# Kernel optimization log

Measured on AMD Instinct MI355X. Metric: run time of the kernel, lower is better.

## Reference

```python
import jax, jax.numpy as jnp
import numpy as np

H = 1024      # hidden_size
E = 8         # num_experts
I = 4 * H     # intermediate_size
B, S = 2, 2048


def setup_inputs() -> dict:
    key = jax.random.key(0)
    ks = jax.random.split(key, 7)
    s_h = 1.0 / np.sqrt(H)
    s_i = 1.0 / np.sqrt(I)
    return {
        "x": jax.random.normal(ks[0], (B, S, H), dtype=jnp.float32),
        "gate_w": jax.random.uniform(ks[1], (H, E), jnp.float32, -s_h, s_h),
        "gate_b": jax.random.uniform(ks[2], (E,), jnp.float32, -s_h, s_h),
        "W1": jax.random.uniform(ks[3], (E, H, I), jnp.float32, -s_h, s_h),
        "b1": jax.random.uniform(ks[4], (E, I), jnp.float32, -s_h, s_h),
        "W2": jax.random.uniform(ks[5], (E, I, H), jnp.float32, -s_i, s_i),
        "b2": jax.random.uniform(ks[6], (E, H), jnp.float32, -s_i, s_i),
    }


def reference(x, gate_w, gate_b, W1, b1, W2, b2):
    b, s, h = x.shape
    flat = x.reshape(-1, h)                      # [T, H]
    T = flat.shape[0]
    e = gate_b.shape[0]

    # Router: softmax -> top-2 -> renormalize
    logits = flat @ gate_w + gate_b              # [T, E]
    probs = jax.nn.softmax(logits, axis=-1)
    top_w, top_idx = jax.lax.top_k(probs, 2)     # [T, 2]
    top_w = top_w / (top_w.sum(axis=-1, keepdims=True) + 1e-6)

    # Dense per-token gate weight matrix [T, E] (0 except top-2 slots)
    gate_full = jnp.zeros((T, e), flat.dtype).at[
        jnp.arange(T)[:, None], top_idx
    ].add(top_w)

    # All experts on all tokens (dense, math-equivalent combine via gate_full)
    hmid = jax.nn.gelu(jnp.einsum('th,ehi->eti', flat, W1) + b1[:, None, :],
                       approximate=True)         # [E, T, I]
    y = jnp.einsum('eti,eih->eth', hmid, W2) + b2[:, None, :]  # [E, T, H]
    out = jnp.einsum('te,eth->th', gate_full, y)  # weighted combine
    return out.reshape(b, s, h)
```

## Files before the change

kernel.cpp:

```cpp
#include <hip/hip_runtime.h>
#include <hip/hip_bf16.h>
#include <math.h>

#define H_DIM 1024
#define E_NUM 8
#define I_DIM 4096
#define T_NUM 4096
#define CAP   8192

typedef __attribute__((ext_vector_type(8))) short bf16x8;
typedef __attribute__((ext_vector_type(4))) float f32x4;

__device__ inline unsigned short f2bf(float f) {
  union { __hip_bfloat16 h; unsigned short u; } cv;
  cv.h = __float2bfloat16(f);
  return cv.u;
}

__global__ void router_kernel(const float* __restrict__ x,
                              const float* __restrict__ gw,
                              const float* __restrict__ gb,
                              int* __restrict__ cnt,
                              int* __restrict__ list,
                              float* __restrict__ tokw) {
  const int t = blockIdx.x;
  const int l = threadIdx.x;
  const float* xr = x + (size_t)t * H_DIM;
  float acc[E_NUM];
#pragma unroll
  for (int e = 0; e < E_NUM; ++e) acc[e] = 0.f;
#pragma unroll
  for (int j = 0; j < H_DIM / 64; ++j) {
    const int h = l + j * 64;
    const float xv = xr[h];
    const float4* g = (const float4*)(gw + (size_t)h * E_NUM);
    const float4 g0 = g[0], g1 = g[1];
    acc[0] += xv * g0.x; acc[1] += xv * g0.y; acc[2] += xv * g0.z; acc[3] += xv * g0.w;
    acc[4] += xv * g1.x; acc[5] += xv * g1.y; acc[6] += xv * g1.z; acc[7] += xv * g1.w;
  }
#pragma unroll
  for (int off = 32; off > 0; off >>= 1) {
#pragma unroll
    for (int e = 0; e < E_NUM; ++e) acc[e] += __shfl_down(acc[e], off, 64);
  }
  if (l == 0) {
    float lg[E_NUM], mx = -1e30f;
#pragma unroll
    for (int e = 0; e < E_NUM; ++e) { lg[e] = acc[e] + gb[e]; mx = fmaxf(mx, lg[e]); }
    float p[E_NUM], s = 0.f;
#pragma unroll
    for (int e = 0; e < E_NUM; ++e) { p[e] = expf(lg[e] - mx); s += p[e]; }
    const float inv = 1.f / s;
#pragma unroll
    for (int e = 0; e < E_NUM; ++e) p[e] *= inv;
    int i0 = 0;
#pragma unroll
    for (int e = 1; e < E_NUM; ++e) if (p[e] > p[i0]) i0 = e;
    int i1 = (i0 == 0) ? 1 : 0;
#pragma unroll
    for (int e = 0; e < E_NUM; ++e) if (e != i0 && p[e] > p[i1]) i1 = e;
    const float denom = p[i0] + p[i1] + 1e-6f;
    const float w0 = p[i0] / denom, w1 = p[i1] / denom;
    int pos = atomicAdd(&cnt[i0], 1);
    list[i0 * CAP + pos] = t * 2;
    tokw[t * 2] = w0;
    pos = atomicAdd(&cnt[i1], 1);
    list[i1 * CAP + pos] = t * 2 + 1;
    tokw[t * 2 + 1] = w1;
  }
}

__global__ void scan_kernel(const int* __restrict__ cnt, int* __restrict__ base) {
  if (threadIdx.x == 0 && blockIdx.x == 0) {
    int b = 0;
    for (int e = 0; e < E_NUM; ++e) { base[e] = b; b += cnt[e]; }
  }
}

__launch_bounds__(256)
__global__ void gemm1_kernel(const float* __restrict__ x,
                             const float* __restrict__ W1,
                             const float* __restrict__ b1,
                             const int* __restrict__ cnt,
                             const int* __restrict__ base,
                             const int* __restrict__ list,
                             unsigned short* __restrict__ hmid) {
  const int e = blockIdx.z;
  const int c = cnt[e];
  const int m0 = blockIdx.y * 128;
  if (m0 >= c) return;
  const int n0 = blockIdx.x * 128;

  __shared__ int toks[128];
  __shared__ __align__(16) unsigned short As[128 * 40];
  __shared__ __align__(16) unsigned short Bs[128 * 40];

  const int tid = threadIdx.x;
  if (tid < 128) {
    int idx = m0 + tid; if (idx >= c) idx = c - 1;
    toks[tid] = list[e * CAP + idx] >> 1;
  }
  __syncthreads();

  const int lane = tid & 63;
  const int wave = tid >> 6;
  const int wm = (wave >> 1) * 64;
  const int wn = (wave & 1) * 64;
  const int l16 = lane & 15;
  const int quad = lane >> 4;

  f32x4 acc[16];
#pragma unroll
  for (int i = 0; i < 16; ++i) acc[i] = (f32x4){0.f, 0.f, 0.f, 0.f};

  const float* W1e = W1 + (size_t)e * H_DIM * I_DIM;

  for (int kt = 0; kt < H_DIM / 32; ++kt) {
    const int k0 = kt * 32;
#pragma unroll
    for (int i = 0; i < 2; ++i) {
      const int idx = tid + i * 256;
      const int row = idx >> 2, g = idx & 3;
      const float* src = x + (size_t)toks[row] * H_DIM + k0 + g * 8;
      const float4 v0 = *(const float4*)(src);
      const float4 v1 = *(const float4*)(src + 4);
      unsigned short tmp[8];
      tmp[0] = f2bf(v0.x); tmp[1] = f2bf(v0.y); tmp[2] = f2bf(v0.z); tmp[3] = f2bf(v0.w);
      tmp[4] = f2bf(v1.x); tmp[5] = f2bf(v1.y); tmp[6] = f2bf(v1.z); tmp[7] = f2bf(v1.w);
      *(f32x4*)&As[row * 40 + g * 8] = *(const f32x4*)tmp;
    }
#pragma unroll
    for (int i = 0; i < 2; ++i) {
      const int idx = tid + i * 256;
      const int n = idx & 127, g = idx >> 7;
      const float* src = W1e + (size_t)(k0 + g * 8) * I_DIM + n0 + n;
      unsigned short tmp[8];
#pragma unroll
      for (int kk = 0; kk < 8; ++kk)
        tmp[kk] = f2bf(src[(size_t)kk * I_DIM]);
      *(f32x4*)&Bs[n * 40 + g * 8] = *(const f32x4*)tmp;
    }
    __syncthreads();
    bf16x8 a[4], b[4];
#pragma unroll
    for (int mf = 0; mf < 4; ++mf)
      a[mf] = *(const bf16x8*)&As[(wm + mf * 16 + l16) * 40 + quad * 8];
#pragma unroll
    for (int nf = 0; nf < 4; ++nf)
      b[nf] = *(const bf16x8*)&Bs[(wn + nf * 16 + l16) * 40 + quad * 8];
#pragma unroll
    for (int mf = 0; mf < 4; ++mf)
#pragma unroll
      for (int nf = 0; nf < 4; ++nf)
        acc[mf * 4 + nf] = __builtin_amdgcn_mfma_f32_16x16x32_bf16(
            a[mf], b[nf], acc[mf * 4 + nf], 0, 0, 0);
    __syncthreads();
  }

  const int hb = base[e];
#pragma unroll
  for (int mf = 0; mf < 4; ++mf) {
#pragma unroll
    for (int reg = 0; reg < 4; ++reg) {
      const int row = wm + mf * 16 + quad * 4 + reg;
      const int gr = m0 + row;
      if (gr < c) {
#pragma unroll
        for (int nf = 0; nf < 4; ++nf) {
          const int col = n0 + wn + nf * 16 + l16;
          const float v = acc[mf * 4 + nf][reg] + b1[e * I_DIM + col];
          const float u = v + 0.044715f * v * v * v;
          const float g = 0.5f * v * (1.0f + tanhf(0.7978845608028654f * u));
          hmid[(size_t)(hb + gr) * I_DIM + col] = f2bf(g);
        }
      }
    }
  }
}

__launch_bounds__(256)
__global__ void gemm2_kernel(const unsigned short* __restrict__ hmid,
                             const float* __restrict__ W2,
                             const float* __restrict__ b2,
                             const int* __restrict__ cnt,
                             const int* __restrict__ base,
                             const int* __restrict__ list,
                             const float* __restrict__ tokw,
                             float* __restrict__ out) {
  const int e = blockIdx.z;
  const int c = cnt[e];
  const int m0 = blockIdx.y * 128;
  if (m0 >= c) return;
  const int n0 = blockIdx.x * 128;

  __shared__ int ents[128];
  __shared__ int arow[128];
  __shared__ __align__(16) unsigned short As[128 * 40];
  __shared__ __align__(16) unsigned short Bs[128 * 40];

  const int tid = threadIdx.x;
  const int hb = base[e];
  if (tid < 128) {
    int idx = m0 + tid; if (idx >= c) idx = c - 1;
    ents[tid] = list[e * CAP + idx];
    arow[tid] = hb + idx;
  }
  __syncthreads();

  const int lane = tid & 63;
  const int wave = tid >> 6;
  const int wm = (wave >> 1) * 64;
  const int wn = (wave & 1) * 64;
  const int l16 = lane & 15;
  const int quad = lane >> 4;

  f32x4 acc[16];
#pragma unroll
  for (int i = 0; i < 16; ++i) acc[i] = (f32x4){0.f, 0.f, 0.f, 0.f};

  const float* W2e = W2 + (size_t)e * I_DIM * H_DIM;

  for (int kt = 0; kt < I_DIM / 32; ++kt) {
    const int k0 = kt * 32;
#pragma unroll
    for (int i = 0; i < 2; ++i) {
      const int idx = tid + i * 256;
      const int row = idx >> 2, kg = idx & 3;
      const f32x4 v = *(const f32x4*)(hmid + (size_t)arow[row] * I_DIM + k0 + kg * 8);
      *(f32x4*)&As[row * 40 + kg * 8] = v;
    }
#pragma unroll
    for (int i = 0; i < 2; ++i) {
      const int idx = tid + i * 256;
      const int n = idx & 127, g = idx >> 7;
      const float* src = W2e + (size_t)(k0 + g * 8) * H_DIM + n0 + n;
      unsigned short tmp[8];
#pragma unroll
      for (int kk = 0; kk < 8; ++kk)
        tmp[kk] = f2bf(src[(size_t)kk * H_DIM]);
      *(f32x4*)&Bs[n * 40 + g * 8] = *(const f32x4*)tmp;
    }
    __syncthreads();
    bf16x8 a[4], b[4];
#pragma unroll
    for (int mf = 0; mf < 4; ++mf)
      a[mf] = *(const bf16x8*)&As[(wm + mf * 16 + l16) * 40 + quad * 8];
#pragma unroll
    for (int nf = 0; nf < 4; ++nf)
      b[nf] = *(const bf16x8*)&Bs[(wn + nf * 16 + l16) * 40 + quad * 8];
#pragma unroll
    for (int mf = 0; mf < 4; ++mf)
#pragma unroll
      for (int nf = 0; nf < 4; ++nf)
        acc[mf * 4 + nf] = __builtin_amdgcn_mfma_f32_16x16x32_bf16(
            a[mf], b[nf], acc[mf * 4 + nf], 0, 0, 0);
    __syncthreads();
  }

#pragma unroll
  for (int mf = 0; mf < 4; ++mf) {
#pragma unroll
    for (int reg = 0; reg < 4; ++reg) {
      const int row = wm + mf * 16 + quad * 4 + reg;
      const int gr = m0 + row;
      if (gr < c) {
        const int ent = ents[row];
        const int t = ent >> 1;
        const float wgt = tokw[ent];
#pragma unroll
        for (int nf = 0; nf < 4; ++nf) {
          const int col = n0 + wn + nf * 16 + l16;
          const float v = acc[mf * 4 + nf][reg] + b2[e * H_DIM + col];
          atomicAdd(&out[(size_t)t * H_DIM + col], wgt * v);
        }
      }
    }
  }
}

extern "C" void kernel_launch(void* const* d_in, const int* in_sizes, int n_in,
                              void* d_out, int out_size, void* d_ws, size_t ws_size,
                              hipStream_t stream) {
  (void)in_sizes; (void)n_in; (void)ws_size;
  const float* x  = (const float*)d_in[0];
  const float* gw = (const float*)d_in[1];
  const float* gb = (const float*)d_in[2];
  const float* W1 = (const float*)d_in[3];
  const float* b1 = (const float*)d_in[4];
  const float* W2 = (const float*)d_in[5];
  const float* b2 = (const float*)d_in[6];
  float* out = (float*)d_out;

  char* w = (char*)d_ws;
  int* cnt   = (int*)w;
  int* base  = (int*)(w + 32);
  int* list  = (int*)(w + 256);
  float* tokw = (float*)(w + 256 + CAP * E_NUM * 4);
  unsigned short* hmid = (unsigned short*)(w + 295168);

  hipMemsetAsync(cnt, 0, 32, stream);
  hipMemsetAsync(out, 0, (size_t)out_size * sizeof(float), stream);

  router_kernel<<<T_NUM, 64, 0, stream>>>(x, gw, gb, cnt, list, tokw);
  scan_kernel<<<1, 64, 0, stream>>>(cnt, base);
  gemm1_kernel<<<dim3(I_DIM / 128, CAP / 128, E_NUM), 256, 0, stream>>>(
      x, W1, b1, cnt, base, list, hmid);
  gemm2_kernel<<<dim3(H_DIM / 128, CAP / 128, E_NUM), 256, 0, stream>>>(
      hmid, W2, b2, cnt, base, list, tokw, out);
}
```

Measured before the change: 750.9 us.

## Pre-convert weights to transposed bf16 and stream tiles via global_load_lds

Adds kernels that convert x to bf16 and transpose-convert W1/W2 into K-contiguous bf16 layouts in workspace. The GEMMs then load A/B tiles straight into LDS with global_load_lds, removing the strided fp32 gathers and per-element conversion from the inner loop. It also swaps tanh-GELU for an equivalent exp-based sigmoid form. The cost is an extra pass over the full weights on every call and a larger workspace requirement, with the old path kept as a fallback when the workspace is too small.

```diff
diff --git a/kernel.cpp b/kernel.cpp
--- a/kernel.cpp
+++ b/kernel.cpp
@@ -10,6 +10,9 @@
 
 typedef __attribute__((ext_vector_type(8))) short bf16x8;
 typedef __attribute__((ext_vector_type(4))) float f32x4;
+
+typedef const __attribute__((address_space(1))) void* gptr_t;
+typedef __attribute__((address_space(3))) void* lptr_t;
 
 __device__ inline unsigned short f2bf(float f) {
   union { __hip_bfloat16 h; unsigned short u; } cv;
@@ -78,13 +81,59 @@
 }
 
 __launch_bounds__(256)
-__global__ void gemm1_kernel(const float* __restrict__ x,
-                             const float* __restrict__ W1,
-                             const float* __restrict__ b1,
-                             const int* __restrict__ cnt,
-                             const int* __restrict__ base,
-                             const int* __restrict__ list,
-                             unsigned short* __restrict__ hmid) {
+__global__ void cvt_x_kernel(const float* __restrict__ x, unsigned short* __restrict__ xb) {
+  const size_t i = ((size_t)blockIdx.x * 256 + threadIdx.x) * 8;
+  const float4 v0 = *(const float4*)(x + i);
+  const float4 v1 = *(const float4*)(x + i + 4);
+  unsigned short t[8];
+  t[0] = f2bf(v0.x); t[1] = f2bf(v0.y); t[2] = f2bf(v0.z); t[3] = f2bf(v0.w);
+  t[4] = f2bf(v1.x); t[5] = f2bf(v1.y); t[6] = f2bf(v1.z); t[7] = f2bf(v1.w);
+  *(f32x4*)(xb + i) = *(const f32x4*)t;
+}
+
+__launch_bounds__(256)
+__global__ void transpose_cvt_kernel(const float* __restrict__ src,
+                                     unsigned short* __restrict__ dst,
+                                     int R, int C) {
+  const int e = blockIdx.z;
+  const int r0 = blockIdx.y * 32;
+  const int c0 = blockIdx.x * 128;
+  const float* s = src + (size_t)e * R * C;
+  unsigned short* d = dst + (size_t)e * R * C;
+  __shared__ unsigned short Lt[32 * 130];
+  const int tid = threadIdx.x;
+#pragma unroll
+  for (int m = 0; m < 4; ++m) {
+    const int li = tid + m * 256;
+    const int r = li >> 5;
+    const int cg = (li & 31) * 4;
+    const float4 v = *(const float4*)(s + (size_t)(r0 + r) * C + c0 + cg);
+    Lt[r * 130 + cg + 0] = f2bf(v.x);
+    Lt[r * 130 + cg + 1] = f2bf(v.y);
+    Lt[r * 130 + cg + 2] = f2bf(v.z);
+    Lt[r * 130 + cg + 3] = f2bf(v.w);
+  }
+  __syncthreads();
+#pragma unroll
+  for (int m = 0; m < 2; ++m) {
+    const int li = tid + m * 256;
+    const int col = li >> 2;
+    const int rg = (li & 3) * 8;
+    unsigned short tmp[8];
+#pragma unroll
+    for (int j = 0; j < 8; ++j) tmp[j] = Lt[(rg + j) * 130 + col];
+    *(f32x4*)(d + (size_t)(c0 + col) * R + r0 + rg) = *(const f32x4*)tmp;
+  }
+}
+
+__launch_bounds__(256)
+__global__ void gemm1_pre_kernel(const unsigned short* __restrict__ xb,
+                                 const unsigned short* __restrict__ W1t,
+                                 const float* __restrict__ b1,
+                                 const int* __restrict__ cnt,
+                                 const int* __restrict__ base,
+                                 const int* __restrict__ list,
+                                 unsigned short* __restrict__ hmid) {
   const int e = blockIdx.z;
   const int c = cnt[e];
   const int m0 = blockIdx.y * 128;
@@ -92,8 +141,8 @@
   const int n0 = blockIdx.x * 128;
 
   __shared__ int toks[128];
-  __shared__ __align__(16) unsigned short As[128 * 40];
-  __shared__ __align__(16) unsigned short Bs[128 * 40];
+  __shared__ __align__(16) unsigned short As[128 * 32];
+  __shared__ __align__(16) unsigned short Bs[128 * 32];
 
   const int tid = threadIdx.x;
   if (tid < 128) {
@@ -109,12 +158,193 @@
   const int l16 = lane & 15;
   const int quad = lane >> 4;
 
+  const int rA0 = tid >> 2;
+  const int rA1 = rA0 + 64;
+  const int kg0 = (tid & 3) * 8;
+  const unsigned short* W1e = W1t + (size_t)e * H_DIM * I_DIM;
+
+  const unsigned short* aSrc0 = xb + (size_t)toks[rA0] * H_DIM + kg0;
+  const unsigned short* aSrc1 = xb + (size_t)toks[rA1] * H_DIM + kg0;
+  const unsigned short* bSrc0 = W1e + (size_t)(n0 + rA0) * H_DIM + kg0;
+  const unsigned short* bSrc1 = W1e + (size_t)(n0 + rA1) * H_DIM + kg0;
+  char* aDst0 = (char*)As + wave * 1024;
+  char* aDst1 = (char*)As + 4096 + wave * 1024;
+  char* bDst0 = (char*)Bs + wave * 1024;
+  char* bDst1 = (char*)Bs + 4096 + wave * 1024;
+
   f32x4 acc[16];
 #pragma unroll
   for (int i = 0; i < 16; ++i) acc[i] = (f32x4){0.f, 0.f, 0.f, 0.f};
 
+  for (int k0 = 0; k0 < H_DIM; k0 += 32) {
+    __builtin_amdgcn_global_load_lds((gptr_t)(aSrc0 + k0), (lptr_t)aDst0, 16, 0, 0);
+    __builtin_amdgcn_global_load_lds((gptr_t)(aSrc1 + k0), (lptr_t)aDst1, 16, 0, 0);
+    __builtin_amdgcn_global_load_lds((gptr_t)(bSrc0 + k0), (lptr_t)bDst0, 16, 0, 0);
+    __builtin_amdgcn_global_load_lds((gptr_t)(bSrc1 + k0), (lptr_t)bDst1, 16, 0, 0);
+    __syncthreads();
+    bf16x8 a[4], b[4];
+#pragma unroll
+    for (int mf = 0; mf < 4; ++mf)
+      a[mf] = *(const bf16x8*)&As[(wm + mf * 16 + l16) * 32 + quad * 8];
+#pragma unroll
+    for (int nf = 0; nf < 4; ++nf)
+      b[nf] = *(const bf16x8*)&Bs[(wn + nf * 16 + l16) * 32 + quad * 8];
+#pragma unroll
+    for (int mf = 0; mf < 4; ++mf)
+#pragma unroll
+      for (int nf = 0; nf < 4; ++nf)
+        acc[mf * 4 + nf] = __builtin_amdgcn_mfma_f32_16x16x32_bf16(
+            a[mf], b[nf], acc[mf * 4 + nf], 0, 0, 0);
+    __syncthreads();
+  }
+
+  const int hb = base[e];
+#pragma unroll
+  for (int mf = 0; mf < 4; ++mf) {
+#pragma unroll
+    for (int reg = 0; reg < 4; ++reg) {
+      const int row = wm + mf * 16 + quad * 4 + reg;
+      const int gr = m0 + row;
+      if (gr < c) {
+#pragma unroll
+        for (int nf = 0; nf < 4; ++nf) {
+          const int col = n0 + wn + nf * 16 + l16;
+          const float v = acc[mf * 4 + nf][reg] + b1[e * I_DIM + col];
+          const float u = v + 0.044715f * v * v * v;
+          const float g = v / (1.f + __expf(-1.5957691216057308f * u));
+          hmid[(size_t)(hb + gr) * I_DIM + col] = f2bf(g);
+        }
+      }
+    }
+  }
+}
+
+__launch_bounds__(256)
+__global__ void gemm2_pre_kernel(const unsigned short* __restrict__ hmid,
+                                 const unsigned short* __restrict__ W2t,
+                                 const float* __restrict__ b2,
+                                 const int* __restrict__ cnt,
+                                 const int* __restrict__ base,
+                                 const int* __restrict__ list,
+                                 const float* __restrict__ tokw,
+                                 float* __restrict__ out) {
+  const int e = blockIdx.z;
+  const int c = cnt[e];
+  const int m0 = blockIdx.y * 128;
+  if (m0 >= c) return;
+  const int n0 = blockIdx.x * 128;
+
+  __shared__ int ents[128];
+  __shared__ int arow[128];
+  __shared__ __align__(16) unsigned short As[128 * 32];
+  __shared__ __align__(16) unsigned short Bs[128 * 32];
+
+  const int tid = threadIdx.x;
+  const int hb = base[e];
+  if (tid < 128) {
+    int idx = m0 + tid; if (idx >= c) idx = c - 1;
+    ents[tid] = list[e * CAP + idx];
+    arow[tid] = hb + idx;
+  }
+  __syncthreads();
+
+  const int lane = tid & 63;
+  const int wave = tid >> 6;
+  const int wm = (wave >> 1) * 64;
+  const int wn = (wave & 1) * 64;
+  const int l16 = lane & 15;
+  const int quad = lane >> 4;
+
+  const int rA0 = tid >> 2;
+  const int rA1 = rA0 + 64;
+  const int kg0 = (tid & 3) * 8;
+  const unsigned short* W2e = W2t + (size_t)e * I_DIM * H_DIM;
+
+  const unsigned short* aSrc0 = hmid + (size_t)arow[rA0] * I_DIM + kg0;
+  const unsigned short* aSrc1 = hmid + (size_t)arow[rA1] * I_DIM + kg0;
+  const unsigned short* bSrc0 = W2e + (size_t)(n0 + rA0) * I_DIM + kg0;
+  const unsigned short* bSrc1 = W2e + (size_t)(n0 + rA1) * I_DIM + kg0;
+  char* aDst0 = (char*)As + wave * 1024;
+  char* aDst1 = (char*)As + 4096 + wave * 1024;
+  char* bDst0 = (char*)Bs + wave * 1024;
+  char* bDst1 = (char*)Bs + 4096 + wave * 1024;
+
+  f32x4 acc[16];
+#pragma unroll
+  for (int i = 0; i < 16; ++i) acc[i] = (f32x4){0.f, 0.f, 0.f, 0.f};
+
+  for (int k0 = 0; k0 < I_DIM; k0 += 32) {
+    __builtin_amdgcn_global_load_lds((gptr_t)(aSrc0 + k0), (lptr_t)aDst0, 16, 0, 0);
+    __builtin_amdgcn_global_load_lds((gptr_t)(aSrc1 + k0), (lptr_t)aDst1, 16, 0, 0);
+    __builtin_amdgcn_global_load_lds((gptr_t)(bSrc0 + k0), (lptr_t)bDst0, 16, 0, 0);
+    __builtin_amdgcn_global_load_lds((gptr_t)(bSrc1 + k0), (lptr_t)bDst1, 16, 0, 0);
+    __syncthreads();
+    bf16x8 a[4], b[4];
+#pragma unroll
+    for (int mf = 0; mf < 4; ++mf)
+      a[mf] = *(const bf16x8*)&As[(wm + mf * 16 + l16) * 32 + quad * 8];
+#pragma unroll
+    for (int nf = 0; nf < 4; ++nf)
+      b[nf] = *(const bf16x8*)&Bs[(wn + nf * 16 + l16) * 32 + quad * 8];
+#pragma unroll
+    for (int mf = 0; mf < 4; ++mf)
+#pragma unroll
+      for (int nf = 0; nf < 4; ++nf)
+        acc[mf * 4 + nf] = __builtin_amdgcn_mfma_f32_16x16x32_bf16(
+            a[mf], b[nf], acc[mf * 4 + nf], 0, 0, 0);
+    __syncthreads();
+  }
+
+#pragma unroll
+  for (int mf = 0; mf < 4; ++mf) {
+#pragma unroll
+    for (int reg = 0; reg < 4; ++reg) {
+      const int row = wm + mf * 16 + quad * 4 + reg;
+      const int gr = m0 + row;
+      if (gr < c) {
+        const int ent = ents[row];
+        const int t = ent >> 1;
+        const float wgt = tokw[ent];
+#pragma unroll
+        for (int nf = 0; nf < 4; ++nf) {
+          const int col = n0 + wn + nf * 16 + l16;
+          const float v = acc[mf * 4 + nf][reg] + b2[e * H_DIM + col];
+          atomicAdd(&out[(size_t)t * H_DIM + col], wgt * v);
+        }
+      }
+    }
+  }
+}
+
+__launch_bounds__(256)
+__global__ void gemm1_fb_kernel(const float* __restrict__ x,
+                                const float* __restrict__ W1,
+                                const float* __restrict__ b1,
+                                const int* __restrict__ cnt,
+                                const int* __restrict__ base,
+                                const int* __restrict__ list,
+                                unsigned short* __restrict__ hmid) {
+  const int e = blockIdx.z;
+  const int c = cnt[e];
+  const int m0 = blockIdx.y * 128;
+  if (m0 >= c) return;
+  const int n0 = blockIdx.x * 128;
+  __shared__ int toks[128];
+  __shared__ __align__(16) unsigned short As[128 * 40];
+  __shared__ __align__(16) unsigned short Bs[128 * 40];
+  const int tid = threadIdx.x;
+  if (tid < 128) {
+    int idx = m0 + tid; if (idx >= c) idx = c - 1;
+    toks[tid] = list[e * CAP + idx] >> 1;
+  }
+  __syncthreads();
+  const int lane = tid & 63, wave = tid >> 6;
+  const int wm = (wave >> 1) * 64, wn = (wave & 1) * 64;
+  const int l16 = lane & 15, quad = lane >> 4;
+  f32x4 acc[16];
+#pragma unroll
+  for (int i = 0; i < 16; ++i) acc[i] = (f32x4){0.f, 0.f, 0.f, 0.f};
   const float* W1e = W1 + (size_t)e * H_DIM * I_DIM;
-
   for (int kt = 0; kt < H_DIM / 32; ++kt) {
     const int k0 = kt * 32;
 #pragma unroll
@@ -136,8 +366,7 @@
       const float* src = W1e + (size_t)(k0 + g * 8) * I_DIM + n0 + n;
       unsigned short tmp[8];
 #pragma unroll
-      for (int kk = 0; kk < 8; ++kk)
-        tmp[kk] = f2bf(src[(size_t)kk * I_DIM]);
+      for (int kk = 0; kk < 8; ++kk) tmp[kk] = f2bf(src[(size_t)kk * I_DIM]);
       *(f32x4*)&Bs[n * 40 + g * 8] = *(const f32x4*)tmp;
     }
     __syncthreads();
@@ -156,10 +385,9 @@
             a[mf], b[nf], acc[mf * 4 + nf], 0, 0, 0);
     __syncthreads();
   }
-
   const int hb = base[e];
 #pragma unroll
-  for (int mf = 0; mf < 4; ++mf) {
+  for (int mf = 0; mf < 4; ++mf)
 #pragma unroll
     for (int reg = 0; reg < 4; ++reg) {
       const int row = wm + mf * 16 + quad * 4 + reg;
@@ -170,34 +398,31 @@
           const int col = n0 + wn + nf * 16 + l16;
           const float v = acc[mf * 4 + nf][reg] + b1[e * I_DIM + col];
           const float u = v + 0.044715f * v * v * v;
-          const float g = 0.5f * v * (1.0f + tanhf(0.7978845608028654f * u));
+          const float g = v / (1.f + __expf(-1.5957691216057308f * u));
           hmid[(size_t)(hb + gr) * I_DIM + col] = f2bf(g);
         }
       }
     }
-  }
 }
 
 __launch_bounds__(256)
-__global__ void gemm2_kernel(const unsigned short* __restrict__ hmid,
-                             const float* __restrict__ W2,
-                             const float* __restrict__ b2,
-                             const int* __restrict__ cnt,
-                             const int* __restrict__ base,
-                             const int* __restrict__ list,
-                             const float* __restrict__ tokw,
-                             float* __restrict__ out) {
+__global__ void gemm2_fb_kernel(const unsigned short* __restrict__ hmid,
+                                const float* __restrict__ W2,
+                                const float* __restrict__ b2,
+                                const int* __restrict__ cnt,
+                                const int* __restrict__ base,
+                                const int* __restrict__ list,
+                                const float* __restrict__ tokw,
+                                float* __restrict__ out) {
   const int e = blockIdx.z;
   const int c = cnt[e];
   const int m0 = blockIdx.y * 128;
   if (m0 >= c) return;
   const int n0 = blockIdx.x * 128;
-
   __shared__ int ents[128];
   __shared__ int arow[128];
   __shared__ __align__(16) unsigned short As[128 * 40];
   __shared__ __align__(16) unsigned short Bs[128 * 40];
-
   const int tid = threadIdx.x;
   const int hb = base[e];
   if (tid < 128) {
@@ -206,20 +431,13 @@
     arow[tid] = hb + idx;
   }
   __syncthreads();
-
-  const int lane = tid & 63;
-  const int wave = tid >> 6;
-  const int wm = (wave >> 1) * 64;
-  const int wn = (wave & 1) * 64;
-  const int l16 = lane & 15;
-  const int quad = lane >> 4;
-
+  const int lane = tid & 63, wave = tid >> 6;
+  const int wm = (wave >> 1) * 64, wn = (wave & 1) * 64;
+  const int l16 = lane & 15, quad = lane >> 4;
   f32x4 acc[16];
 #pragma unroll
   for (int i = 0; i < 16; ++i) acc[i] = (f32x4){0.f, 0.f, 0.f, 0.f};
-
   const float* W2e = W2 + (size_t)e * I_DIM * H_DIM;
-
   for (int kt = 0; kt < I_DIM / 32; ++kt) {
     const int k0 = kt * 32;
 #pragma unroll
@@ -236,8 +454,7 @@
       const float* src = W2e + (size_t)(k0 + g * 8) * H_DIM + n0 + n;
       unsigned short tmp[8];
 #pragma unroll
-      for (int kk = 0; kk < 8; ++kk)
-        tmp[kk] = f2bf(src[(size_t)kk * H_DIM]);
+      for (int kk = 0; kk < 8; ++kk) tmp[kk] = f2bf(src[(size_t)kk * H_DIM]);
       *(f32x4*)&Bs[n * 40 + g * 8] = *(const f32x4*)tmp;
     }
     __syncthreads();
@@ -256,9 +473,8 @@
             a[mf], b[nf], acc[mf * 4 + nf], 0, 0, 0);
     __syncthreads();
   }
-
-#pragma unroll
-  for (int mf = 0; mf < 4; ++mf) {
+#pragma unroll
+  for (int mf = 0; mf < 4; ++mf)
 #pragma unroll
     for (int reg = 0; reg < 4; ++reg) {
       const int row = wm + mf * 16 + quad * 4 + reg;
@@ -275,13 +491,12 @@
         }
       }
     }
-  }
 }
 
 extern "C" void kernel_launch(void* const* d_in, const int* in_sizes, int n_in,
                               void* d_out, int out_size, void* d_ws, size_t ws_size,
                               hipStream_t stream) {
-  (void)in_sizes; (void)n_in; (void)ws_size;
+  (void)in_sizes; (void)n_in;
   const float* x  = (const float*)d_in[0];
   const float* gw = (const float*)d_in[1];
   const float* gb = (const float*)d_in[2];
@@ -292,19 +507,36 @@
   float* out = (float*)d_out;
 
   char* w = (char*)d_ws;
-  int* cnt   = (int*)w;
-  int* base  = (int*)(w + 32);
-  int* list  = (int*)(w + 256);
-  float* tokw = (float*)(w + 256 + CAP * E_NUM * 4);
+  int* cnt    = (int*)w;
+  int* base   = (int*)(w + 32);
+  int* list   = (int*)(w + 256);
+  float* tokw = (float*)(w + 262400);
   unsigned short* hmid = (unsigned short*)(w + 295168);
+  unsigned short* W1t  = (unsigned short*)(w + 67404032);
+  unsigned short* W2t  = (unsigned short*)(w + 134512896);
+  unsigned short* xb   = (unsigned short*)(w + 201621760);
+  const size_t NEED = 210010368;
 
   hipMemsetAsync(cnt, 0, 32, stream);
   hipMemsetAsync(out, 0, (size_t)out_size * sizeof(float), stream);
 
   router_kernel<<<T_NUM, 64, 0, stream>>>(x, gw, gb, cnt, list, tokw);
   scan_kernel<<<1, 64, 0, stream>>>(cnt, base);
-  gemm1_kernel<<<dim3(I_DIM / 128, CAP / 128, E_NUM), 256, 0, stream>>>(
-      x, W1, b1, cnt, base, list, hmid);
-  gemm2_kernel<<<dim3(H_DIM / 128, CAP / 128, E_NUM), 256, 0, stream>>>(
-      hmid, W2, b2, cnt, base, list, tokw, out);
-}
+
+  if (ws_size >= NEED) {
+    cvt_x_kernel<<<T_NUM * H_DIM / 2048, 256, 0, stream>>>(x, xb);
+    transpose_cvt_kernel<<<dim3(I_DIM / 128, H_DIM / 32, E_NUM), 256, 0, stream>>>(
+        W1, W1t, H_DIM, I_DIM);
+    transpose_cvt_kernel<<<dim3(H_DIM / 128, I_DIM / 32, E_NUM), 256, 0, stream>>>(
+        W2, W2t, I_DIM, H_DIM);
+    gemm1_pre_kernel<<<dim3(I_DIM / 128, CAP / 128, E_NUM), 256, 0, stream>>>(
+        xb, W1t, b1, cnt, base, list, hmid);
+    gemm2_pre_kernel<<<dim3(H_DIM / 128, CAP / 128, E_NUM), 256, 0, stream>>>(
+        hmid, W2t, b2, cnt, base, list, tokw, out);
+  } else {
+    gemm1_fb_kernel<<<dim3(I_DIM / 128, CAP / 128, E_NUM), 256, 0, stream>>>(
+        x, W1, b1, cnt, base, list, hmid);
+    gemm2_fb_kernel<<<dim3(H_DIM / 128, CAP / 128, E_NUM), 256, 0, stream>>>(
+        hmid, W2, b2, cnt, base, list, tokw, out);
+  }
+}
```

Result: faster. 691.0 us (-8.0%).
